# Optimization experiments

Measured on AMD Instinct MI355X. Metric: run time of the kernel, lower is better.

The kernel has to match this reference:

```python
import jax, jax.numpy as jnp
import numpy as np

N = 100000
E = 1600000
D_IN = 128
D_OUT = 64
NEG_SLOPE = 0.2
EPS = 1e-10


def setup_inputs() -> dict:
    key = jax.random.key(0)
    k1, k2, k3, k4, k5 = jax.random.split(key, 5)
    x = jax.random.normal(k1, (N, D_IN), dtype=jnp.float32)
    edge_index = jax.random.randint(k2, (2, E), 0, N, dtype=jnp.int64)
    edge_weight = jax.random.uniform(k3, (E,), dtype=jnp.float32)
    # Learned params: Linear weight (stored as [in, out] so Wh = x @ W) and attention vector a [2*out]
    W = jax.random.normal(k4, (D_IN, D_OUT), dtype=jnp.float32) / np.sqrt(D_IN)
    a = jax.random.normal(k5, (2 * D_OUT,), dtype=jnp.float32) * np.sqrt(2.0 / (2 * D_OUT))
    return {"x": x, "edge_index": edge_index, "edge_weight": edge_weight, "W": W, "a": a}


def reference(x, edge_index, edge_weight, W, a):
    n = x.shape[0]
    Wh = x @ W  # [N, D_OUT]
    src, tgt = edge_index[0], edge_index[1]
    # e_ij = LeakyReLU(a^T [Wh_i || Wh_j]) computed without materializing the concat:
    a_src, a_tgt = a[:D_OUT], a[D_OUT:]
    e = (Wh @ a_src)[src] + (Wh @ a_tgt)[tgt]  # [E]
    e = jnp.where(e > 0, e, NEG_SLOPE * e)
    e = e * edge_weight
    # segment softmax over incoming edges of each target node
    e_max = jax.ops.segment_max(e, tgt, num_segments=n)
    e_exp = jnp.exp(e - e_max[tgt])
    e_sum = jax.ops.segment_sum(e_exp, tgt, num_segments=n)
    alpha = e_exp / (e_sum[tgt] + EPS)
    # weighted scatter-add aggregation
    messages = alpha[:, None] * Wh[src]  # [E, D_OUT]
    out = jax.ops.segment_sum(messages, tgt, num_segments=n)
    return out
```

## Files before the change

kernel.cpp:

```cpp
#include <hip/hip_runtime.h>
#include <hip/hip_bf16.h>

#define DOUT 64
#define DIN 128
#define NEG_SLOPE 0.2f
#define EPSV 1e-10f
#define LDA 136
#define BKT_SHIFT 8
#define BKT_SIZE 256
#define NBMAX 512
#define PASSA_CHUNK 2048
#define CAP 12
#define CAP_B 5120

typedef __attribute__((ext_vector_type(8))) __bf16 bf16x8;
typedef __attribute__((ext_vector_type(8))) unsigned short ushortx8;
typedef __attribute__((ext_vector_type(4))) float floatx4;

__device__ __forceinline__ float bf16_to_f32(unsigned short u) {
    return __uint_as_float(((unsigned int)u) << 16);
}
__device__ __forceinline__ unsigned short f32_to_bf16(float f) {
    __hip_bfloat16 h = __float2bfloat16(f);
    unsigned short u;
    __builtin_memcpy(&u, &h, 2);
    return u;
}
__device__ __forceinline__ unsigned int f32x2_to_bf16x2(float a, float b) {
    __hip_bfloat162 h = __float22bfloat162_rn(make_float2(a, b));
    unsigned int u;
    __builtin_memcpy(&u, &h, 4);
    return u;
}
__device__ __forceinline__ float leaky_exp(float vs, float vt, float w) {
    float v = vs + vt;
    v = (v > 0.f) ? v : NEG_SLOPE * v;
    return __expf(v * w);
}

__global__ __launch_bounds__(256) void gat_gemm_scores(
    const float* __restrict__ x, const float* __restrict__ W,
    const float* __restrict__ a, unsigned short* __restrict__ Wh,
    float* __restrict__ ssrc, float* __restrict__ stgt, int N)
{
    __shared__ unsigned short A_sh[64 * LDA];
    __shared__ unsigned short B_sh[64 * LDA];

    const int tid = threadIdx.x;
    const int rowbase = blockIdx.x * 64;

    for (int idx = tid; idx < DIN * DOUT; idx += 256) {
        int k = idx >> 6, n = idx & 63;
        B_sh[n * LDA + k] = f32_to_bf16(W[idx]);
    }
    for (int it = 0; it < 8; ++it) {
        int flat = it * 1024 + tid * 4;
        int row = flat >> 7, k = flat & 127;
        int grow = rowbase + row;
        float4 v = make_float4(0.f, 0.f, 0.f, 0.f);
        if (grow < N) v = *(const float4*)&x[(size_t)grow * DIN + k];
        uint2 packed = make_uint2(f32x2_to_bf16x2(v.x, v.y),
                                  f32x2_to_bf16x2(v.z, v.w));
        *(uint2*)&A_sh[row * LDA + k] = packed;
    }
    __syncthreads();

    const int lane = tid & 63;
    const int wv   = tid >> 6;
    const int c16  = lane & 15;
    const int quad = lane >> 4;

    floatx4 acc[4] = {floatx4{0,0,0,0}, floatx4{0,0,0,0},
                      floatx4{0,0,0,0}, floatx4{0,0,0,0}};

    const int arow = (wv * 16 + c16) * LDA;
    #pragma unroll
    for (int kk = 0; kk < 4; ++kk) {
        const int koff = kk * 32 + quad * 8;
        bf16x8 af = __builtin_bit_cast(bf16x8, *(const ushortx8*)&A_sh[arow + koff]);
        #pragma unroll
        for (int nt = 0; nt < 4; ++nt) {
            bf16x8 bf = __builtin_bit_cast(bf16x8,
                           *(const ushortx8*)&B_sh[(nt * 16 + c16) * LDA + koff]);
            acc[nt] = __builtin_amdgcn_mfma_f32_16x16x32_bf16(af, bf, acc[nt], 0, 0, 0);
        }
    }

    float asrc_v[4], atgt_v[4];
    #pragma unroll
    for (int nt = 0; nt < 4; ++nt) {
        asrc_v[nt] = a[nt * 16 + c16];
        atgt_v[nt] = a[64 + nt * 16 + c16];
    }
    const int rbase = rowbase + wv * 16 + quad * 4;
    #pragma unroll
    for (int r = 0; r < 4; ++r) {
        int row = rbase + r;
        if (row < N) {
            #pragma unroll
            for (int nt = 0; nt < 4; ++nt)
                Wh[(size_t)row * DOUT + nt * 16 + c16] = f32_to_bf16(acc[nt][r]);
        }
    }
    #pragma unroll
    for (int r = 0; r < 4; ++r) {
        float ps = 0.f, pt = 0.f;
        #pragma unroll
        for (int nt = 0; nt < 4; ++nt) {
            ps += acc[nt][r] * asrc_v[nt];
            pt += acc[nt][r] * atgt_v[nt];
        }
        #pragma unroll
        for (int m = 1; m < 16; m <<= 1) {
            ps += __shfl_xor(ps, m);
            pt += __shfl_xor(pt, m);
        }
        if (c16 == 0) {
            int row = rbase + r;
            if (row < N) { ssrc[row] = ps; stgt[row] = pt; }
        }
    }
}

__global__ __launch_bounds__(256) void gat_bin_fused(
    const int* __restrict__ ei, const float* __restrict__ ew,
    const float* __restrict__ ssrc, const float* __restrict__ stgt,
    int* __restrict__ cnt, int2* __restrict__ staged_g, int E)
{
    __shared__ int2 staged[NBMAX * CAP];
    __shared__ int fill[NBMAX];
    __shared__ int gpos[NBMAX];
    const int tid = threadIdx.x;
    for (int bb = tid; bb < NBMAX; bb += 256) fill[bb] = 0;
    __syncthreads();

    const int base = blockIdx.x * PASSA_CHUNK;
    #pragma unroll
    for (int j = 0; j < PASSA_CHUNK / 1024; ++j) {
        int e4 = base + j * 1024 + tid * 4;
        if (e4 + 3 < E) {
            int4 ss = *(const int4*)&ei[e4];
            int4 tt = *(const int4*)&ei[E + e4];
            float4 ww = *(const float4*)&ew[e4];
            float vs0 = ssrc[ss.x], vs1 = ssrc[ss.y], vs2 = ssrc[ss.z], vs3 = ssrc[ss.w];
            float vt0 = stgt[tt.x], vt1 = stgt[tt.y], vt2 = stgt[tt.z], vt3 = stgt[tt.w];
            float pv[4] = {leaky_exp(vs0, vt0, ww.x), leaky_exp(vs1, vt1, ww.y),
                           leaky_exp(vs2, vt2, ww.z), leaky_exp(vs3, vt3, ww.w)};
            int sv[4] = {ss.x, ss.y, ss.z, ss.w};
            int tv[4] = {tt.x, tt.y, tt.z, tt.w};
            #pragma unroll
            for (int u = 0; u < 4; ++u) {
                int b = tv[u] >> BKT_SHIFT;
                int2 rec = make_int2(sv[u] | ((tv[u] & (BKT_SIZE - 1)) << 17),
                                     __float_as_int(pv[u]));
                int pos = atomicAdd(&fill[b], 1);
                if (pos < CAP) staged[b * CAP + pos] = rec;
                else {
                    int gp = atomicAdd(&cnt[b], 1);
                    if (gp < CAP_B) staged_g[(size_t)b * CAP_B + gp] = rec;
                }
            }
        } else {
            for (int e = e4; e < E; ++e) {
                int s = ei[e], t = ei[E + e];
                float p = leaky_exp(ssrc[s], stgt[t], ew[e]);
                int b = t >> BKT_SHIFT;
                int2 rec = make_int2(s | ((t & (BKT_SIZE - 1)) << 17),
                                     __float_as_int(p));
                int pos = atomicAdd(&fill[b], 1);
                if (pos < CAP) staged[b * CAP + pos] = rec;
                else {
                    int gp = atomicAdd(&cnt[b], 1);
                    if (gp < CAP_B) staged_g[(size_t)b * CAP_B + gp] = rec;
                }
            }
        }
    }
    __syncthreads();

    for (int bb = tid; bb < NBMAX; bb += 256) {
        int f = min(fill[bb], CAP);
        gpos[bb] = (f > 0) ? atomicAdd(&cnt[bb], f) : 0;
    }
    __syncthreads();

    for (int i = tid; i < NBMAX * CAP; i += 256) {
        int b = i / CAP;
        int r = i - b * CAP;
        if (r < min(fill[b], CAP)) {
            int gp = gpos[b] + r;
            if (gp < CAP_B) staged_g[(size_t)b * CAP_B + gp] = staged[i];
        }
    }
}

__global__ __launch_bounds__(256) void gat_binB_sort(
    const int2* __restrict__ staged_g, const int* __restrict__ cnt,
    int* __restrict__ rbeg, int* __restrict__ rend,
    int2* __restrict__ sorted_sp, int N)
{
    __shared__ int lcnt[BKT_SIZE];
    __shared__ int lcur[BKT_SIZE];
    __shared__ int lscan[BKT_SIZE];

    const int b = blockIdx.x;
    const int tid = threadIdx.x;
    const int base = b * CAP_B;
    const int n = min(cnt[b], CAP_B);

    lcnt[tid] = 0;
    __syncthreads();

    for (int i = tid; i < n; i += 256)
        atomicAdd(&lcnt[(staged_g[base + i].x >> 17) & (BKT_SIZE - 1)], 1);
    __syncthreads();

    int c = lcnt[tid];
    lscan[tid] = c;
    __syncthreads();
    for (int off = 1; off < 256; off <<= 1) {
        int t = (tid >= off) ? lscan[tid - off] : 0;
        __syncthreads();
        lscan[tid] += t;
        __syncthreads();
    }
    int excl = lscan[tid] - c;
    lcur[tid] = excl;

    int g = (b << BKT_SHIFT) + tid;
    if (g < N) { rbeg[g] = base + excl; rend[g] = base + excl + c; }
    __syncthreads();

    for (int i = tid; i < n; i += 256) {
        int2 rec = staged_g[base + i];
        int tl = (rec.x >> 17) & (BKT_SIZE - 1);
        int pos = atomicAdd(&lcur[tl], 1);
        sorted_sp[base + pos] = make_int2(rec.x & 0x1FFFF, rec.y);
    }
}

__global__ __launch_bounds__(256) void gat_aggregate_csr(
    const int* __restrict__ rbeg, const int* __restrict__ rend,
    const int2* __restrict__ sorted_sp,
    const unsigned short* __restrict__ Wh, float* __restrict__ out, int N)
{
    int t = blockIdx.x * 4 + (threadIdx.x >> 6);
    if (t >= N) return;
    int lane = threadIdx.x & 63;
    int sub  = lane >> 3;
    int c8   = lane & 7;

    int beg = rbeg[t], end = rend[t];

    float acc[8] = {0.f, 0.f, 0.f, 0.f, 0.f, 0.f, 0.f, 0.f};
    float psum = 0.f;

    int i = beg + sub;
    for (; i + 8 < end; i += 16) {
        int2 spA = sorted_sp[i];
        int2 spB = sorted_sp[i + 8];
        float pA = __int_as_float(spA.y);
        float pB = __int_as_float(spB.y);
        ushortx8 wA = *(const ushortx8*)&Wh[(size_t)spA.x * DOUT + c8 * 8];
        ushortx8 wB = *(const ushortx8*)&Wh[(size_t)spB.x * DOUT + c8 * 8];
        #pragma unroll
        for (int j = 0; j < 8; ++j) acc[j] += pA * bf16_to_f32(wA[j]);
        psum += pA;
        #pragma unroll
        for (int j = 0; j < 8; ++j) acc[j] += pB * bf16_to_f32(wB[j]);
        psum += pB;
    }
    if (i < end) {
        int2 sp = sorted_sp[i];
        float p = __int_as_float(sp.y);
        ushortx8 w = *(const ushortx8*)&Wh[(size_t)sp.x * DOUT + c8 * 8];
        #pragma unroll
        for (int j = 0; j < 8; ++j) acc[j] += p * bf16_to_f32(w[j]);
        psum += p;
    }

    #pragma unroll
    for (int m = 8; m < 64; m <<= 1) {
        #pragma unroll
        for (int j = 0; j < 8; ++j) acc[j] += __shfl_xor(acc[j], m);
        psum += __shfl_xor(psum, m);
    }

    if (sub == 0) {
        float inv = 1.0f / (psum + EPSV);
        float4 o0 = make_float4(acc[0] * inv, acc[1] * inv, acc[2] * inv, acc[3] * inv);
        float4 o1 = make_float4(acc[4] * inv, acc[5] * inv, acc[6] * inv, acc[7] * inv);
        *(float4*)&out[(size_t)t * DOUT + c8 * 8]     = o0;
        *(float4*)&out[(size_t)t * DOUT + c8 * 8 + 4] = o1;
    }
}

extern "C" void kernel_launch(void* const* d_in, const int* in_sizes, int n_in,
                              void* d_out, int out_size, void* d_ws, size_t ws_size,
                              hipStream_t stream) {
    const float* x  = (const float*)d_in[0];
    const int*   ei = (const int*)d_in[1];
    const float* ew = (const float*)d_in[2];
    const float* W  = (const float*)d_in[3];
    const float* a  = (const float*)d_in[4];
    const int N = in_sizes[0] / DIN;
    const int E = in_sizes[2];
    float* out = (float*)d_out;

    const int nbk = (N + BKT_SIZE - 1) >> BKT_SHIFT;

    char* wsb = (char*)d_ws;
    unsigned short* Wh = (unsigned short*)wsb;      wsb += (size_t)N * DOUT * 2;
    float* ssrc      = (float*)wsb;                 wsb += (size_t)N * 4;
    float* stgt      = (float*)wsb;                 wsb += (size_t)N * 4;
    int*   rbeg      = (int*)wsb;                   wsb += (size_t)N * 4;
    int*   rend      = (int*)wsb;                   wsb += (size_t)N * 4;
    int*   cnt       = (int*)wsb;                   wsb += NBMAX * 4;
    wsb = (char*)(((uintptr_t)wsb + 15) & ~(uintptr_t)15);
    int2*  staged_g  = (int2*)wsb;                  wsb += (size_t)nbk * CAP_B * 8;
    int2*  sorted_sp = (int2*)wsb;                  wsb += (size_t)nbk * CAP_B * 8;

    (void)hipMemsetAsync(cnt, 0, NBMAX * sizeof(int), stream);

    gat_gemm_scores<<<(N + 63) / 64, 256, 0, stream>>>(x, W, a, Wh, ssrc, stgt, N);
    gat_bin_fused<<<(E + PASSA_CHUNK - 1) / PASSA_CHUNK, 256, 0, stream>>>(
                  ei, ew, ssrc, stgt, cnt, staged_g, E);
    gat_binB_sort<<<nbk, 256, 0, stream>>>(staged_g, cnt, rbeg, rend, sorted_sp, N);
    gat_aggregate_csr<<<(N + 3) / 4, 256, 0, stream>>>(rbeg, rend, sorted_sp, Wh, out, N);
}
```

Baseline: 212.1 us.

## Replace bucketed staging sort with exact histogram-scan CSR build

Swaps the two-pass bucket staging and per-bucket local sort for a precise CSR construction. A degree histogram is built with global atomics, then a bucket-level scan and a per-node scan, and finally a scatter that computes logits and places each edge directly at its CSR slot through per-node atomic cursors. This removes the fixed-capacity staging buffers and their overflow truncation risk, and removes one full pass over the edge records. In exchange it adds two extra kernel launches, a memset of N ints, and contended global atomics on per-node counters, and it reads the target indices twice.

```diff
diff --git a/kernel.cpp b/kernel.cpp
--- a/kernel.cpp
+++ b/kernel.cpp
@@ -9,9 +9,6 @@
 #define BKT_SHIFT 8
 #define BKT_SIZE 256
 #define NBMAX 512
-#define PASSA_CHUNK 2048
-#define CAP 12
-#define CAP_B 5120
 
 typedef __attribute__((ext_vector_type(8))) __bf16 bf16x8;
 typedef __attribute__((ext_vector_type(8))) unsigned short ushortx8;
@@ -122,100 +119,63 @@
     }
 }
 
-__global__ __launch_bounds__(256) void gat_bin_fused(
-    const int* __restrict__ ei, const float* __restrict__ ew,
-    const float* __restrict__ ssrc, const float* __restrict__ stgt,
-    int* __restrict__ cnt, int2* __restrict__ staged_g, int E)
-{
-    __shared__ int2 staged[NBMAX * CAP];
-    __shared__ int fill[NBMAX];
-    __shared__ int gpos[NBMAX];
+__global__ __launch_bounds__(256) void gat_hist(
+    const int* __restrict__ tgt, int* __restrict__ deg,
+    int* __restrict__ cnt, int E)
+{
+    __shared__ int lh[NBMAX];
     const int tid = threadIdx.x;
-    for (int bb = tid; bb < NBMAX; bb += 256) fill[bb] = 0;
-    __syncthreads();
-
-    const int base = blockIdx.x * PASSA_CHUNK;
-    #pragma unroll
-    for (int j = 0; j < PASSA_CHUNK / 1024; ++j) {
-        int e4 = base + j * 1024 + tid * 4;
-        if (e4 + 3 < E) {
-            int4 ss = *(const int4*)&ei[e4];
-            int4 tt = *(const int4*)&ei[E + e4];
-            float4 ww = *(const float4*)&ew[e4];
-            float vs0 = ssrc[ss.x], vs1 = ssrc[ss.y], vs2 = ssrc[ss.z], vs3 = ssrc[ss.w];
-            float vt0 = stgt[tt.x], vt1 = stgt[tt.y], vt2 = stgt[tt.z], vt3 = stgt[tt.w];
-            float pv[4] = {leaky_exp(vs0, vt0, ww.x), leaky_exp(vs1, vt1, ww.y),
-                           leaky_exp(vs2, vt2, ww.z), leaky_exp(vs3, vt3, ww.w)};
-            int sv[4] = {ss.x, ss.y, ss.z, ss.w};
-            int tv[4] = {tt.x, tt.y, tt.z, tt.w};
-            #pragma unroll
-            for (int u = 0; u < 4; ++u) {
-                int b = tv[u] >> BKT_SHIFT;
-                int2 rec = make_int2(sv[u] | ((tv[u] & (BKT_SIZE - 1)) << 17),
-                                     __float_as_int(pv[u]));
-                int pos = atomicAdd(&fill[b], 1);
-                if (pos < CAP) staged[b * CAP + pos] = rec;
-                else {
-                    int gp = atomicAdd(&cnt[b], 1);
-                    if (gp < CAP_B) staged_g[(size_t)b * CAP_B + gp] = rec;
-                }
-            }
-        } else {
-            for (int e = e4; e < E; ++e) {
-                int s = ei[e], t = ei[E + e];
-                float p = leaky_exp(ssrc[s], stgt[t], ew[e]);
-                int b = t >> BKT_SHIFT;
-                int2 rec = make_int2(s | ((t & (BKT_SIZE - 1)) << 17),
-                                     __float_as_int(p));
-                int pos = atomicAdd(&fill[b], 1);
-                if (pos < CAP) staged[b * CAP + pos] = rec;
-                else {
-                    int gp = atomicAdd(&cnt[b], 1);
-                    if (gp < CAP_B) staged_g[(size_t)b * CAP_B + gp] = rec;
-                }
-            }
-        }
-    }
-    __syncthreads();
-
-    for (int bb = tid; bb < NBMAX; bb += 256) {
-        int f = min(fill[bb], CAP);
-        gpos[bb] = (f > 0) ? atomicAdd(&cnt[bb], f) : 0;
-    }
-    __syncthreads();
-
-    for (int i = tid; i < NBMAX * CAP; i += 256) {
-        int b = i / CAP;
-        int r = i - b * CAP;
-        if (r < min(fill[b], CAP)) {
-            int gp = gpos[b] + r;
-            if (gp < CAP_B) staged_g[(size_t)b * CAP_B + gp] = staged[i];
-        }
-    }
-}
-
-__global__ __launch_bounds__(256) void gat_binB_sort(
-    const int2* __restrict__ staged_g, const int* __restrict__ cnt,
-    int* __restrict__ rbeg, int* __restrict__ rend,
-    int2* __restrict__ sorted_sp, int N)
-{
-    __shared__ int lcnt[BKT_SIZE];
-    __shared__ int lcur[BKT_SIZE];
+    for (int i = tid; i < NBMAX; i += 256) lh[i] = 0;
+    __syncthreads();
+
+    int e4 = blockIdx.x * 1024 + tid * 4;
+    if (e4 + 3 < E) {
+        int4 tt = *(const int4*)&tgt[e4];
+        atomicAdd(&deg[tt.x], 1);
+        atomicAdd(&deg[tt.y], 1);
+        atomicAdd(&deg[tt.z], 1);
+        atomicAdd(&deg[tt.w], 1);
+        atomicAdd(&lh[tt.x >> BKT_SHIFT], 1);
+        atomicAdd(&lh[tt.y >> BKT_SHIFT], 1);
+        atomicAdd(&lh[tt.z >> BKT_SHIFT], 1);
+        atomicAdd(&lh[tt.w >> BKT_SHIFT], 1);
+    } else {
+        for (int e = e4; e < E; ++e) {
+            int t = tgt[e];
+            atomicAdd(&deg[t], 1);
+            atomicAdd(&lh[t >> BKT_SHIFT], 1);
+        }
+    }
+    __syncthreads();
+    for (int i = tid; i < NBMAX; i += 256)
+        if (lh[i] > 0) atomicAdd(&cnt[i], lh[i]);
+}
+
+__global__ __launch_bounds__(256) void gat_bscan(
+    const int* __restrict__ cnt, int* __restrict__ bbase)
+{
+    __shared__ int lds[NBMAX];
+    const int tid = threadIdx.x;
+    for (int i = tid; i < NBMAX; i += 256) lds[i] = cnt[i];
+    __syncthreads();
+    if (tid == 0) {
+        int acc = 0;
+        for (int j = 0; j < NBMAX; ++j) { int c = lds[j]; lds[j] = acc; acc += c; }
+    }
+    __syncthreads();
+    for (int i = tid; i < NBMAX; i += 256) bbase[i] = lds[i];
+}
+
+__global__ __launch_bounds__(256) void gat_rscan(
+    const int* __restrict__ deg, const int* __restrict__ bbase,
+    int* __restrict__ rbeg, int* __restrict__ cur, int N)
+{
     __shared__ int lscan[BKT_SIZE];
-
     const int b = blockIdx.x;
     const int tid = threadIdx.x;
-    const int base = b * CAP_B;
-    const int n = min(cnt[b], CAP_B);
-
-    lcnt[tid] = 0;
-    __syncthreads();
-
-    for (int i = tid; i < n; i += 256)
-        atomicAdd(&lcnt[(staged_g[base + i].x >> 17) & (BKT_SIZE - 1)], 1);
-    __syncthreads();
-
-    int c = lcnt[tid];
+    const int g = (b << BKT_SHIFT) + tid;
+
+    int c = (g < N) ? deg[g] : 0;
     lscan[tid] = c;
     __syncthreads();
     for (int off = 1; off < 256; off <<= 1) {
@@ -225,17 +185,41 @@
         __syncthreads();
     }
     int excl = lscan[tid] - c;
-    lcur[tid] = excl;
-
-    int g = (b << BKT_SHIFT) + tid;
-    if (g < N) { rbeg[g] = base + excl; rend[g] = base + excl + c; }
-    __syncthreads();
-
-    for (int i = tid; i < n; i += 256) {
-        int2 rec = staged_g[base + i];
-        int tl = (rec.x >> 17) & (BKT_SIZE - 1);
-        int pos = atomicAdd(&lcur[tl], 1);
-        sorted_sp[base + pos] = make_int2(rec.x & 0x1FFFF, rec.y);
+    if (g < N) {
+        int p = bbase[b] + excl;
+        rbeg[g] = p;
+        cur[g]  = p;
+    }
+}
+
+__global__ __launch_bounds__(256) void gat_scatter_logits(
+    const int* __restrict__ ei, const float* __restrict__ ew,
+    const float* __restrict__ ssrc, const float* __restrict__ stgt,
+    int* __restrict__ cur, int2* __restrict__ sorted_sp, int E)
+{
+    int e4 = blockIdx.x * 1024 + threadIdx.x * 4;
+    if (e4 + 3 < E) {
+        int4 ss = *(const int4*)&ei[e4];
+        int4 tt = *(const int4*)&ei[E + e4];
+        float4 ww = *(const float4*)&ew[e4];
+        float vs0 = ssrc[ss.x], vs1 = ssrc[ss.y], vs2 = ssrc[ss.z], vs3 = ssrc[ss.w];
+        float vt0 = stgt[tt.x], vt1 = stgt[tt.y], vt2 = stgt[tt.z], vt3 = stgt[tt.w];
+        float pv[4] = {leaky_exp(vs0, vt0, ww.x), leaky_exp(vs1, vt1, ww.y),
+                       leaky_exp(vs2, vt2, ww.z), leaky_exp(vs3, vt3, ww.w)};
+        int sv[4] = {ss.x, ss.y, ss.z, ss.w};
+        int tv[4] = {tt.x, tt.y, tt.z, tt.w};
+        #pragma unroll
+        for (int u = 0; u < 4; ++u) {
+            int pos = atomicAdd(&cur[tv[u]], 1);
+            sorted_sp[pos] = make_int2(sv[u], __float_as_int(pv[u]));
+        }
+    } else {
+        for (int e = e4; e < E; ++e) {
+            int s = ei[e], t = ei[E + e];
+            float p = leaky_exp(ssrc[s], stgt[t], ew[e]);
+            int pos = atomicAdd(&cur[t], 1);
+            sorted_sp[pos] = make_int2(s, __float_as_int(p));
+        }
     }
 }
 
@@ -313,18 +297,24 @@
     unsigned short* Wh = (unsigned short*)wsb;      wsb += (size_t)N * DOUT * 2;
     float* ssrc      = (float*)wsb;                 wsb += (size_t)N * 4;
     float* stgt      = (float*)wsb;                 wsb += (size_t)N * 4;
+    int*   deg       = (int*)wsb;                   wsb += (size_t)N * 4;
     int*   rbeg      = (int*)wsb;                   wsb += (size_t)N * 4;
-    int*   rend      = (int*)wsb;                   wsb += (size_t)N * 4;
+    int*   cur       = (int*)wsb;                   wsb += (size_t)N * 4;
     int*   cnt       = (int*)wsb;                   wsb += NBMAX * 4;
+    int*   bbase     = (int*)wsb;                   wsb += NBMAX * 4;
     wsb = (char*)(((uintptr_t)wsb + 15) & ~(uintptr_t)15);
-    int2*  staged_g  = (int2*)wsb;                  wsb += (size_t)nbk * CAP_B * 8;
-    int2*  sorted_sp = (int2*)wsb;                  wsb += (size_t)nbk * CAP_B * 8;
-
+    int2*  sorted_sp = (int2*)wsb;                  wsb += (size_t)E * 8;
+
+    (void)hipMemsetAsync(deg, 0, (size_t)N * sizeof(int), stream);
     (void)hipMemsetAsync(cnt, 0, NBMAX * sizeof(int), stream);
 
+    const int egrid = (E + 1023) / 1024;
     gat_gemm_scores<<<(N + 63) / 64, 256, 0, stream>>>(x, W, a, Wh, ssrc, stgt, N);
-    gat_bin_fused<<<(E + PASSA_CHUNK - 1) / PASSA_CHUNK, 256, 0, stream>>>(
-                  ei, ew, ssrc, stgt, cnt, staged_g, E);
-    gat_binB_sort<<<nbk, 256, 0, stream>>>(staged_g, cnt, rbeg, rend, sorted_sp, N);
-    gat_aggregate_csr<<<(N + 3) / 4, 256, 0, stream>>>(rbeg, rend, sorted_sp, Wh, out, N);
-}
+    gat_hist<<<egrid, 256, 0, stream>>>(ei + E, deg, cnt, E);
+    gat_bscan<<<1, 256, 0, stream>>>(cnt, bbase);
+    gat_rscan<<<nbk, 256, 0, stream>>>(deg, bbase, rbeg, cur, N);
+    gat_scatter_logits<<<egrid, 256, 0, stream>>>(ei, ew, ssrc, stgt, cur,
+                                                  sorted_sp, E);
+    gat_aggregate_csr<<<(N + 3) / 4, 256, 0, stream>>>(rbeg, cur, sorted_sp,
+                                                       Wh, out, N);
+}
```

New measurement: 336.2 us. 58.5% more time.
